# Kernel optimization log

Measured on AMD Instinct MI355X. Metric: run time of the kernel, lower is better.

The kernel has to match this reference:

```python
import jax, jax.numpy as jnp
import numpy as np

B_SCALE = 1.3195079565048218
N_LEVELS = 16
BASE_RES = 16
MAX_PARAMS = 2 ** 19
N_POINTS = 1048576
PRIMES = (1, 2654435761, 805459861)  # uint32 hash primes (Instant-NGP)


def _level_meta():
    offsets, sizes, inds = [], [], []
    off = 0
    for i in range(N_LEVELS):
        res = int(np.ceil(BASE_RES * np.exp(i * np.log(B_SCALE)) - 1.0)) + 1
        p = res ** 3
        if p % 8 != 0:
            p = ((p + 7) // 8) * 8
        p = min(MAX_PARAMS, p)
        offsets.append(off)
        sizes.append(p)
        inds.append(res ** 3 <= p)  # dense (under_hash) vs hashed level
        off += p
    return offsets, sizes, inds, off


OFFSETS, SIZES, INDICATORS, TOTAL_PARAMS = _level_meta()
TOTAL_HASH_SIZE = TOTAL_PARAMS * 2  # == 11445040


def _encode_level(x01, table2, level):
    # x01: [N,3] in [0,1]; table2: [total_params, 2]
    scale = np.float32(BASE_RES * np.exp(level * np.log(B_SCALE)) - 1.0)
    resolution = np.uint32(np.ceil(scale) + 1)
    map_size = np.uint32(SIZES[level])
    pos = x01 * scale + 0.5
    grid_f = jnp.floor(pos)
    frac = pos - grid_f                           # [N,3] trilinear weights
    grid = grid_f.astype(jnp.uint32)              # [N,3]
    feat = jnp.zeros((x01.shape[0], 2), dtype=table2.dtype)
    primes = np.array(PRIMES, dtype=np.uint32)
    stride = np.array([1, int(resolution), int(resolution) * int(resolution)], dtype=np.uint32)
    for idx in range(8):  # 8 grid corners
        sel = np.array([(idx >> d) & 1 for d in range(3)], dtype=np.uint32)
        corner = grid + sel                       # [N,3] uint32
        w = jnp.prod(jnp.where(sel[None, :] == 1, frac, 1.0 - frac), axis=-1)  # [N]
        if INDICATORS[level]:
            c = corner * stride[None, :]
            h = c[:, 0] + c[:, 1] + c[:, 2]       # under_hash (dense indexing)
        else:
            c = corner * primes[None, :]          # uint32 wraparound multiply
            h = c[:, 0] ^ c[:, 1] ^ c[:, 2]       # fast_hash
        index = (h % map_size).astype(jnp.int32) + np.int32(OFFSETS[level])
        feat = feat + w[:, None] * table2[index]  # gather + trilinear blend
    return feat


def setup_inputs() -> dict:
    key = jax.random.key(0)
    k1, k2 = jax.random.split(key)
    positions = jax.random.uniform(k1, (N_POINTS, 3), dtype=jnp.float32, minval=-1.0, maxval=1.0)
    # random_initialize: (rand*2-1)*1e-4
    hash_table = jax.random.uniform(k2, (TOTAL_HASH_SIZE,), dtype=jnp.float32, minval=-1e-4, maxval=1e-4)
    return {"positions": positions, "hash_table": hash_table}


def reference(positions, hash_table):
    x01 = (positions + 1.0) * 0.5  # bound = 1
    table2 = hash_table.reshape(-1, 2)
    feats = [_encode_level(x01, table2, l) for l in range(N_LEVELS)]
    return jnp.concatenate(feats, axis=-1)  # [N, 32]
```

## Files before the change

### kernel.cpp

```cpp
#include <hip/hip_runtime.h>
#include <math.h>
#include <stdint.h>

#define NLV 16
#define NDENSE 6
#define NHASH 10
#define NMERGE 6
#define SORT_RES 32
#define NBINS (SORT_RES * SORT_RES * SORT_RES)

typedef float evf2 __attribute__((ext_vector_type(2)));
typedef unsigned int evu4 __attribute__((ext_vector_type(4)));
typedef _Float16 evh2 __attribute__((ext_vector_type(2)));
typedef _Float16 evh4 __attribute__((ext_vector_type(4)));

struct Params {
  float scale[NLV];
  uint32_t res[NLV];
  uint32_t msize[NLV];
  uint32_t offset[NLV];
};

struct ParamsD {
  float scale[NDENSE];
  uint32_t res[NDENSE];
  uint32_t msize[NDENSE];
  uint32_t offset[NDENSE];
};

struct ParamsH {
  float scale[NMERGE];
  uint32_t offset[NMERGE];
};

__device__ __forceinline__ float ntload(const float* p) {
  return __builtin_nontemporal_load(p);
}

__device__ __forceinline__ int xcd_swz(int bid, int nwg) {
  int q = nwg >> 3, r = nwg & 7;
  int x = bid & 7, i = bid >> 3;
  return (x < r ? x * (q + 1) : r * (q + 1) + (x - r) * q) + i;
}

__device__ __forceinline__ uint32_t cell_key(float xr, float yr, float zr) {
  float x01 = (xr + 1.0f) * 0.5f;
  float y01 = (yr + 1.0f) * 0.5f;
  float z01 = (zr + 1.0f) * 0.5f;
  int cx = (int)(x01 * (float)SORT_RES);
  int cy = (int)(y01 * (float)SORT_RES);
  int cz = (int)(z01 * (float)SORT_RES);
  cx = cx < 0 ? 0 : (cx > SORT_RES-1 ? SORT_RES-1 : cx);
  cy = cy < 0 ? 0 : (cy > SORT_RES-1 ? SORT_RES-1 : cy);
  cz = cz < 0 ? 0 : (cz > SORT_RES-1 ? SORT_RES-1 : cz);
  return (uint32_t)(cx | (cy << 5) | (cz << 10));
}

__global__ __launch_bounds__(256) void zero_bins_kernel(uint32_t* bins) {
  int i = blockIdx.x * 256 + threadIdx.x;
  if (i < NBINS) bins[i] = 0u;
}

__global__ __launch_bounds__(256) void hist_kernel(
    const float* __restrict__ positions, uint32_t* __restrict__ bins, int n) {
  int t = blockIdx.x * 256 + threadIdx.x;
  int p0 = t * 4;
  if (p0 >= n) return;
  const float4 A = *reinterpret_cast<const float4*>(positions + 3*p0);
  const float4 B = *reinterpret_cast<const float4*>(positions + 3*p0 + 4);
  const float4 C = *reinterpret_cast<const float4*>(positions + 3*p0 + 8);
  atomicAdd(&bins[cell_key(A.x, A.y, A.z)], 1u);
  atomicAdd(&bins[cell_key(A.w, B.x, B.y)], 1u);
  atomicAdd(&bins[cell_key(B.z, B.w, C.x)], 1u);
  atomicAdd(&bins[cell_key(C.y, C.z, C.w)], 1u);
}

__global__ __launch_bounds__(1024) void scan_kernel(
    const uint32_t* __restrict__ bins, uint32_t* __restrict__ cursor) {
  __shared__ uint32_t lds[1024];
  int t = threadIdx.x;
  uint32_t local[32];
  uint32_t s = 0;
  #pragma unroll
  for (int j = 0; j < 32; ++j) { local[j] = bins[t*32 + j]; s += local[j]; }
  lds[t] = s;
  __syncthreads();
  for (int off = 1; off < 1024; off <<= 1) {
    uint32_t v = (t >= off) ? lds[t - off] : 0u;
    __syncthreads();
    lds[t] += v;
    __syncthreads();
  }
  uint32_t run = lds[t] - s;
  #pragma unroll
  for (int j = 0; j < 32; ++j) { cursor[t*32 + j] = run; run += local[j]; }
}

__global__ __launch_bounds__(256) void scatter_kernel(
    const float* __restrict__ positions, uint32_t* __restrict__ cursor,
    evu4* __restrict__ spi, int n) {
  int t = blockIdx.x * 256 + threadIdx.x;
  int p0 = t * 4;
  if (p0 >= n) return;
  const float4 A = *reinterpret_cast<const float4*>(positions + 3*p0);
  const float4 B = *reinterpret_cast<const float4*>(positions + 3*p0 + 4);
  const float4 C = *reinterpret_cast<const float4*>(positions + 3*p0 + 8);
  float xs[4] = {A.x, A.w, B.z, C.y};
  float ys[4] = {A.y, B.x, B.w, C.z};
  float zs[4] = {A.z, B.y, C.x, C.w};
  #pragma unroll
  for (int q = 0; q < 4; ++q) {
    uint32_t k = cell_key(xs[q], ys[q], zs[q]);
    uint32_t dst = atomicAdd(&cursor[k], 1u);
    evu4 v;
    v.x = __float_as_uint(xs[q]);
    v.y = __float_as_uint(ys[q]);
    v.z = __float_as_uint(zs[q]);
    v.w = (uint32_t)(p0 + q);
    spi[dst] = v;
  }
}

__device__ __forceinline__ void hash_feat(
    float x01, float y01, float z01, float scale, uint32_t mask,
    const float* __restrict__ tbl, float& f0, float& f1)
{
  float px = x01 * scale + 0.5f;
  float py = y01 * scale + 0.5f;
  float pz = z01 * scale + 0.5f;
  float fx = floorf(px), fy = floorf(py), fz = floorf(pz);
  float tx = px - fx, ty = py - fy, tz = pz - fz;
  uint32_t gx = (uint32_t)fx, gy = (uint32_t)fy, gz = (uint32_t)fz;

  float wxa = 1.0f - tx, wxb = tx;
  float wy_[2] = {1.0f - ty, ty};
  float wz_[2] = {1.0f - tz, tz};

  f0 = 0.0f; f1 = 0.0f;
  if ((gx & 1u) == 0u) {
    #pragma unroll
    for (int cyz = 0; cyz < 4; ++cyz) {
      uint32_t cy = gy + (cyz & 1u);
      uint32_t cz = gz + (cyz >> 1);
      uint32_t hy = (cy * 2654435761u) ^ (cz * 805459861u);
      uint32_t ha = (gx ^ hy) & mask;
      float wyz = wy_[cyz & 1u] * wz_[cyz >> 1];
      float wa = wxa * wyz, wb = wxb * wyz;
      const float4 t4 = *reinterpret_cast<const float4*>(tbl + 2u * (ha & ~1u));
      float2 ta, tb;
      if (ha & 1u) { ta.x = t4.z; ta.y = t4.w; tb.x = t4.x; tb.y = t4.y; }
      else         { ta.x = t4.x; ta.y = t4.y; tb.x = t4.z; tb.y = t4.w; }
      f0 += wa * ta.x; f1 += wa * ta.y;
      f0 += wb * tb.x; f1 += wb * tb.y;
    }
  } else {
    #pragma unroll
    for (int cyz = 0; cyz < 4; ++cyz) {
      uint32_t cy = gy + (cyz & 1u);
      uint32_t cz = gz + (cyz >> 1);
      uint32_t hy = (cy * 2654435761u) ^ (cz * 805459861u);
      uint32_t ha = (gx ^ hy) & mask;
      uint32_t hb = ((gx + 1u) ^ hy) & mask;
      float wyz = wy_[cyz & 1u] * wz_[cyz >> 1];
      float wa = wxa * wyz, wb = wxb * wyz;
      const float2 ta = *reinterpret_cast<const float2*>(tbl + 2u * ha);
      const float2 tb = *reinterpret_cast<const float2*>(tbl + 2u * hb);
      f0 += wa * ta.x; f1 += wa * ta.y;
      f0 += wb * tb.x; f1 += wb * tb.y;
    }
  }
}

__global__ __launch_bounds__(256) void hash_multi_kernel(
    const evu4* __restrict__ spi,
    const float* __restrict__ table,
    evh2* __restrict__ tmpH,
    ParamsH ph, uint32_t mask, int n)
{
  int bid = xcd_swz(blockIdx.x, gridDim.x);
  int t = bid * 256 + threadIdx.x;
  int p0 = t * 2;
  if (p0 >= n) return;

  evu4 a = __builtin_nontemporal_load(spi + p0);
  evu4 b = __builtin_nontemporal_load(spi + p0 + 1);
  float x0 = (__uint_as_float(a.x) + 1.0f) * 0.5f;
  float y0 = (__uint_as_float(a.y) + 1.0f) * 0.5f;
  float z0 = (__uint_as_float(a.z) + 1.0f) * 0.5f;
  float x1 = (__uint_as_float(b.x) + 1.0f) * 0.5f;
  float y1 = (__uint_as_float(b.y) + 1.0f) * 0.5f;
  float z1 = (__uint_as_float(b.z) + 1.0f) * 0.5f;

  #pragma unroll
  for (int l = 0; l < NMERGE; ++l) {
    const float s = ph.scale[l];
    const float* __restrict__ tbl = table + 2u * ph.offset[l];
    float f00, f01, f10, f11;
    hash_feat(x0, y0, z0, s, mask, tbl, f00, f01);
    hash_feat(x1, y1, z1, s, mask, tbl, f10, f11);
    evh4 v;
    v.x = (_Float16)f00; v.y = (_Float16)f01;
    v.z = (_Float16)f10; v.w = (_Float16)f11;
    __builtin_nontemporal_store(v,
        reinterpret_cast<evh4*>(tmpH + (size_t)l * n + p0));
  }
}

__global__ __launch_bounds__(256) void hash_level_kernel(
    const evu4* __restrict__ spi,
    const float* __restrict__ tbl,
    evh2* __restrict__ tmpH,
    float scale, uint32_t mask, int n)
{
  int bid = xcd_swz(blockIdx.x, gridDim.x);
  int t = bid * 256 + threadIdx.x;
  int p0 = t * 2;
  if (p0 >= n) return;

  evu4 a = __builtin_nontemporal_load(spi + p0);
  evu4 b = __builtin_nontemporal_load(spi + p0 + 1);
  float f00, f01, f10, f11;
  hash_feat((__uint_as_float(a.x) + 1.0f) * 0.5f,
            (__uint_as_float(a.y) + 1.0f) * 0.5f,
            (__uint_as_float(a.z) + 1.0f) * 0.5f, scale, mask, tbl, f00, f01);
  hash_feat((__uint_as_float(b.x) + 1.0f) * 0.5f,
            (__uint_as_float(b.y) + 1.0f) * 0.5f,
            (__uint_as_float(b.z) + 1.0f) * 0.5f, scale, mask, tbl, f10, f11);
  evh4 v;
  v.x = (_Float16)f00; v.y = (_Float16)f01;
  v.z = (_Float16)f10; v.w = (_Float16)f11;
  __builtin_nontemporal_store(v, reinterpret_cast<evh4*>(tmpH + p0));
}

#define PBS 128
__global__ __launch_bounds__(PBS) void dense_pack2_kernel(
    const evu4* __restrict__ spi,
    const float* __restrict__ table,
    const evh2* __restrict__ tmpH,
    float* __restrict__ out,
    ParamsD prm, int n)
{
  __shared__ float lds[PBS * 33];
  __shared__ uint32_t lds_oi[PBS];
  int t = threadIdx.x;
  int base = xcd_swz(blockIdx.x, gridDim.x) * PBS;
  int p = base + t;

  if (p < n) {
    evu4 a = __builtin_nontemporal_load(spi + p);
    float x = (__uint_as_float(a.x) + 1.0f) * 0.5f;
    float y = (__uint_as_float(a.y) + 1.0f) * 0.5f;
    float z = (__uint_as_float(a.z) + 1.0f) * 0.5f;
    lds_oi[t] = a.w;

    #pragma unroll
    for (int l = 0; l < NDENSE; ++l) {
      const float s = prm.scale[l];
      const uint32_t res = prm.res[l];
      const uint32_t ms = prm.msize[l];
      const float* __restrict__ tbl = table + 2u * prm.offset[l];
      const uint32_t res2 = res * res;

      float px = x * s + 0.5f;
      float py = y * s + 0.5f;
      float pz = z * s + 0.5f;
      float fx = floorf(px), fy = floorf(py), fz = floorf(pz);
      float tx = px - fx, ty = py - fy, tz = pz - fz;
      uint32_t gx = (uint32_t)fx, gy = (uint32_t)fy, gz = (uint32_t)fz;

      float wxa = 1.0f - tx, wxb = tx;
      float wy_[2] = {1.0f - ty, ty};
      float wz_[2] = {1.0f - tz, tz};

      float f0 = 0.0f, f1 = 0.0f;
      #pragma unroll
      for (int cyz = 0; cyz < 4; ++cyz) {
        uint32_t cy = gy + (cyz & 1u);
        uint32_t cz = gz + ((cyz >> 1) & 1u);
        uint32_t h = gx + cy * res + cz * res2;
        if (h >= ms) h -= ms;
        float wyz = wy_[cyz & 1u] * wz_[(cyz >> 1) & 1u];
        float2 ta, tb;
        if (h + 1u < ms) {
          const float4 t4 = *reinterpret_cast<const float4*>(tbl + 2u * h);
          ta.x = t4.x; ta.y = t4.y; tb.x = t4.z; tb.y = t4.w;
        } else {
          ta = *reinterpret_cast<const float2*>(tbl + 2u * h);
          tb = *reinterpret_cast<const float2*>(tbl);
        }
        float wa = wxa * wyz, wb = wxb * wyz;
        f0 += wa * ta.x; f1 += wa * ta.y;
        f0 += wb * tb.x; f1 += wb * tb.y;
      }
      lds[t*33 + 2*l]     = f0;
      lds[t*33 + 2*l + 1] = f1;
    }

    #pragma unroll
    for (int j = 0; j < NHASH; ++j) {
      evh2 v = __builtin_nontemporal_load(tmpH + (size_t)j * n + p);
      lds[t*33 + 12 + 2*j]     = (float)v.x;
      lds[t*33 + 12 + 2*j + 1] = (float)v.y;
    }
  }
  __syncthreads();

  if (base + PBS <= n) {
    int qr = t >> 3, r = t & 7;
    #pragma unroll
    for (int k = 0; k < 8; ++k) {
      int q = k * (PBS/8) + qr;
      uint32_t oi = lds_oi[q];
      float4 v = make_float4(lds[q*33 + r*4], lds[q*33 + r*4 + 1],
                             lds[q*33 + r*4 + 2], lds[q*33 + r*4 + 3]);
      reinterpret_cast<float4*>(out + (size_t)oi * 32u)[r] = v;
    }
  } else if (p < n) {
    uint32_t oi = lds_oi[t];
    float4* o = reinterpret_cast<float4*>(out + (size_t)oi * 32u);
    #pragma unroll
    for (int k = 0; k < 8; ++k)
      o[k] = make_float4(lds[t*33 + 4*k], lds[t*33 + 4*k + 1],
                         lds[t*33 + 4*k + 2], lds[t*33 + 4*k + 3]);
  }
}

__global__ __launch_bounds__(256) void hash_enc_kernel(
    const float* __restrict__ positions,
    const float* __restrict__ table,
    float* __restrict__ out,
    Params prm, int n)
{
  int p = blockIdx.x * 256 + threadIdx.x;
  if (p >= n) return;

  float x = (positions[3*p+0] + 1.0f) * 0.5f;
  float y = (positions[3*p+1] + 1.0f) * 0.5f;
  float z = (positions[3*p+2] + 1.0f) * 0.5f;

  float acc[32];

  #pragma unroll
  for (int l = 0; l < NLV; ++l) {
    const float s = prm.scale[l];
    const uint32_t res = prm.res[l];
    const uint32_t ms = prm.msize[l];
    const uint32_t off = prm.offset[l];
    float px = x * s + 0.5f;
    float py = y * s + 0.5f;
    float pz = z * s + 0.5f;
    float fx = floorf(px), fy = floorf(py), fz = floorf(pz);
    float tx = px - fx, ty = py - fy, tz = pz - fz;
    uint32_t gx = (uint32_t)fx, gy = (uint32_t)fy, gz = (uint32_t)fz;
    float wx[2] = {1.0f - tx, tx};
    float wy[2] = {1.0f - ty, ty};
    float wz[2] = {1.0f - tz, tz};
    float f0 = 0.0f, f1 = 0.0f;
    #pragma unroll
    for (int c = 0; c < 8; ++c) {
      uint32_t cx = gx + (c & 1u);
      uint32_t cy = gy + ((c >> 1) & 1u);
      uint32_t cz = gz + ((c >> 2) & 1u);
      uint32_t h;
      if (l < NDENSE) {
        h = cx + cy * res + cz * res * res;
        if (h >= ms) h -= ms;
      } else {
        h = cx ^ (cy * 2654435761u) ^ (cz * 805459861u);
        h &= (ms - 1u);
      }
      float w = (wx[c & 1u] * wy[(c >> 1) & 1u]) * wz[(c >> 2) & 1u];
      const float2 t = *reinterpret_cast<const float2*>(table + 2u * (h + off));
      f0 += w * t.x;
      f1 += w * t.y;
    }
    acc[2*l]   = f0;
    acc[2*l+1] = f1;
  }

  float4* o = reinterpret_cast<float4*>(out + (size_t)p * 32u);
  #pragma unroll
  for (int k = 0; k < 8; ++k)
    o[k] = make_float4(acc[4*k+0], acc[4*k+1], acc[4*k+2], acc[4*k+3]);
}

extern "C" void kernel_launch(void* const* d_in, const int* in_sizes, int n_in,
                              void* d_out, int out_size, void* d_ws, size_t ws_size,
                              hipStream_t stream) {
  const float* positions = (const float*)d_in[0];
  const float* table     = (const float*)d_in[1];
  float* out             = (float*)d_out;
  int n = in_sizes[0] / 3;

  Params prm;
  const double lnb = log(1.3195079565048218);
  uint32_t off = 0;
  for (int l = 0; l < NLV; ++l) {
    double sd = 16.0 * exp((double)l * lnb) - 1.0;
    uint32_t res_meta = (uint32_t)ceil(sd) + 1u;
    uint64_t p3 = (uint64_t)res_meta * res_meta * res_meta;
    uint64_t ps = (p3 % 8ull) ? ((p3 + 7ull) / 8ull) * 8ull : p3;
    if (ps > (1ull << 19)) ps = 1ull << 19;
    float sf = (float)sd;
    uint32_t res_enc = (uint32_t)(ceilf(sf) + 1.0f);
    prm.scale[l]  = sf;
    prm.res[l]    = res_enc;
    prm.msize[l]  = (uint32_t)ps;
    prm.offset[l] = off;
    off += (uint32_t)ps;
  }
  ParamsD pd;
  for (int l = 0; l < NDENSE; ++l) {
    pd.scale[l] = prm.scale[l]; pd.res[l] = prm.res[l];
    pd.msize[l] = prm.msize[l]; pd.offset[l] = prm.offset[l];
  }
  ParamsH ph;
  for (int l = 0; l < NMERGE; ++l) {
    ph.scale[l]  = prm.scale[NDENSE + l];
    ph.offset[l] = prm.offset[NDENSE + l];
  }

  dim3 block(256);
  dim3 gfull((n + 255) / 256);
  dim3 ghash((n/2 + 255) / 256);
  dim3 gquad((n/4 + 255) / 256);
  dim3 gpack((n + PBS - 1) / PBS);

  size_t tmp_b  = (size_t)NHASH * n * sizeof(evh2);
  size_t sp_off = tmp_b;
  size_t bn_off = sp_off + (size_t)n * sizeof(evu4);
  size_t cu_off = bn_off + (size_t)NBINS * sizeof(uint32_t);
  size_t total  = cu_off + (size_t)NBINS * sizeof(uint32_t);

  char* wsb = (char*)d_ws;

  if (ws_size >= total && (n % 4) == 0) {
    evh2*     tmpH   = (evh2*)wsb;
    evu4*     spi    = (evu4*)(wsb + sp_off);
    uint32_t* bins   = (uint32_t*)(wsb + bn_off);
    uint32_t* cursor = (uint32_t*)(wsb + cu_off);

    hipLaunchKernelGGL(zero_bins_kernel, dim3((NBINS + 255) / 256), block, 0, stream, bins);
    hipLaunchKernelGGL(hist_kernel, gquad, block, 0, stream, positions, bins, n);
    hipLaunchKernelGGL(scan_kernel, dim3(1), dim3(1024), 0, stream, bins, cursor);
    hipLaunchKernelGGL(scatter_kernel, gquad, block, 0, stream,
                       positions, cursor, spi, n);

    hipLaunchKernelGGL(hash_multi_kernel, ghash, block, 0, stream,
                       spi, table, tmpH, ph, prm.msize[NDENSE] - 1u, n);
    for (int l = NDENSE + NMERGE; l < NLV; ++l) {
      hipLaunchKernelGGL(hash_level_kernel, ghash, block, 0, stream,
                         spi, table + 2u * prm.offset[l],
                         tmpH + (size_t)(l - NDENSE) * n,
                         prm.scale[l], prm.msize[l] - 1u, n);
    }
    hipLaunchKernelGGL(dense_pack2_kernel, gpack, dim3(PBS), 0, stream,
                       spi, table, tmpH, out, pd, n);
  } else {
    hipLaunchKernelGGL(hash_enc_kernel, gfull, block, 0, stream,
                       positions, table, out, prm, n);
  }
}
```

Baseline: 432.6 us.

## Fuse last four hashed levels into one kernel, simplify scatter, stream output

Replaces the four separate per-level launches for the finest hashed levels with a single kernel that loops over those levels, reusing the loaded sorted positions and cutting launch and re-read overhead. The scatter kernel now handles one point per thread instead of four, which raises thread count and atomic parallelism but drops the vectorized position loads. The dense pack kernel's final output writes become nontemporal stores. The merged kernel holds more live state per thread and serializes four levels of gathers inside one thread, which may lower occupancy and reduce latency hiding.

```diff
diff --git a/kernel.cpp b/kernel.cpp
--- a/kernel.cpp
+++ b/kernel.cpp
@@ -6,10 +6,12 @@
 #define NDENSE 6
 #define NHASH 10
 #define NMERGE 6
+#define NMERGE2 4
 #define SORT_RES 32
 #define NBINS (SORT_RES * SORT_RES * SORT_RES)
 
 typedef float evf2 __attribute__((ext_vector_type(2)));
+typedef float evf4 __attribute__((ext_vector_type(4)));
 typedef unsigned int evu4 __attribute__((ext_vector_type(4)));
 typedef _Float16 evh2 __attribute__((ext_vector_type(2)));
 typedef _Float16 evh4 __attribute__((ext_vector_type(4)));
@@ -33,9 +35,10 @@
   uint32_t offset[NMERGE];
 };
 
-__device__ __forceinline__ float ntload(const float* p) {
-  return __builtin_nontemporal_load(p);
-}
+struct ParamsH2 {
+  float scale[NMERGE2];
+  uint32_t offset[NMERGE2];
+};
 
 __device__ __forceinline__ int xcd_swz(int bid, int nwg) {
   int q = nwg >> 3, r = nwg & 7;
@@ -99,26 +102,17 @@
 __global__ __launch_bounds__(256) void scatter_kernel(
     const float* __restrict__ positions, uint32_t* __restrict__ cursor,
     evu4* __restrict__ spi, int n) {
-  int t = blockIdx.x * 256 + threadIdx.x;
-  int p0 = t * 4;
-  if (p0 >= n) return;
-  const float4 A = *reinterpret_cast<const float4*>(positions + 3*p0);
-  const float4 B = *reinterpret_cast<const float4*>(positions + 3*p0 + 4);
-  const float4 C = *reinterpret_cast<const float4*>(positions + 3*p0 + 8);
-  float xs[4] = {A.x, A.w, B.z, C.y};
-  float ys[4] = {A.y, B.x, B.w, C.z};
-  float zs[4] = {A.z, B.y, C.x, C.w};
-  #pragma unroll
-  for (int q = 0; q < 4; ++q) {
-    uint32_t k = cell_key(xs[q], ys[q], zs[q]);
-    uint32_t dst = atomicAdd(&cursor[k], 1u);
-    evu4 v;
-    v.x = __float_as_uint(xs[q]);
-    v.y = __float_as_uint(ys[q]);
-    v.z = __float_as_uint(zs[q]);
-    v.w = (uint32_t)(p0 + q);
-    spi[dst] = v;
-  }
+  int p = blockIdx.x * 256 + threadIdx.x;
+  if (p >= n) return;
+  float x = positions[3*p], y = positions[3*p+1], z = positions[3*p+2];
+  uint32_t k = cell_key(x, y, z);
+  uint32_t dst = atomicAdd(&cursor[k], 1u);
+  evu4 v;
+  v.x = __float_as_uint(x);
+  v.y = __float_as_uint(y);
+  v.z = __float_as_uint(z);
+  v.w = (uint32_t)p;
+  spi[dst] = v;
 }
 
 __device__ __forceinline__ void hash_feat(
@@ -206,11 +200,11 @@
   }
 }
 
-__global__ __launch_bounds__(256) void hash_level_kernel(
+__global__ __launch_bounds__(256) void hash_multi2_kernel(
     const evu4* __restrict__ spi,
-    const float* __restrict__ tbl,
+    const float* __restrict__ table,
     evh2* __restrict__ tmpH,
-    float scale, uint32_t mask, int n)
+    ParamsH2 ph, uint32_t mask, int n)
 {
   int bid = xcd_swz(blockIdx.x, gridDim.x);
   int t = bid * 256 + threadIdx.x;
@@ -219,17 +213,26 @@
 
   evu4 a = __builtin_nontemporal_load(spi + p0);
   evu4 b = __builtin_nontemporal_load(spi + p0 + 1);
-  float f00, f01, f10, f11;
-  hash_feat((__uint_as_float(a.x) + 1.0f) * 0.5f,
-            (__uint_as_float(a.y) + 1.0f) * 0.5f,
-            (__uint_as_float(a.z) + 1.0f) * 0.5f, scale, mask, tbl, f00, f01);
-  hash_feat((__uint_as_float(b.x) + 1.0f) * 0.5f,
-            (__uint_as_float(b.y) + 1.0f) * 0.5f,
-            (__uint_as_float(b.z) + 1.0f) * 0.5f, scale, mask, tbl, f10, f11);
-  evh4 v;
-  v.x = (_Float16)f00; v.y = (_Float16)f01;
-  v.z = (_Float16)f10; v.w = (_Float16)f11;
-  __builtin_nontemporal_store(v, reinterpret_cast<evh4*>(tmpH + p0));
+  float x0 = (__uint_as_float(a.x) + 1.0f) * 0.5f;
+  float y0 = (__uint_as_float(a.y) + 1.0f) * 0.5f;
+  float z0 = (__uint_as_float(a.z) + 1.0f) * 0.5f;
+  float x1 = (__uint_as_float(b.x) + 1.0f) * 0.5f;
+  float y1 = (__uint_as_float(b.y) + 1.0f) * 0.5f;
+  float z1 = (__uint_as_float(b.z) + 1.0f) * 0.5f;
+
+  #pragma unroll
+  for (int l = 0; l < NMERGE2; ++l) {
+    const float s = ph.scale[l];
+    const float* __restrict__ tbl = table + 2u * ph.offset[l];
+    float f00, f01, f10, f11;
+    hash_feat(x0, y0, z0, s, mask, tbl, f00, f01);
+    hash_feat(x1, y1, z1, s, mask, tbl, f10, f11);
+    evh4 v;
+    v.x = (_Float16)f00; v.y = (_Float16)f01;
+    v.z = (_Float16)f10; v.w = (_Float16)f11;
+    __builtin_nontemporal_store(v,
+        reinterpret_cast<evh4*>(tmpH + (size_t)(NMERGE + l) * n + p0));
+  }
 }
 
 #define PBS 128
@@ -311,9 +314,11 @@
     for (int k = 0; k < 8; ++k) {
       int q = k * (PBS/8) + qr;
       uint32_t oi = lds_oi[q];
-      float4 v = make_float4(lds[q*33 + r*4], lds[q*33 + r*4 + 1],
-                             lds[q*33 + r*4 + 2], lds[q*33 + r*4 + 3]);
-      reinterpret_cast<float4*>(out + (size_t)oi * 32u)[r] = v;
+      evf4 v;
+      v.x = lds[q*33 + r*4];     v.y = lds[q*33 + r*4 + 1];
+      v.z = lds[q*33 + r*4 + 2]; v.w = lds[q*33 + r*4 + 3];
+      __builtin_nontemporal_store(v,
+          reinterpret_cast<evf4*>(out + (size_t)oi * 32u) + r);
     }
   } else if (p < n) {
     uint32_t oi = lds_oi[t];
@@ -419,6 +424,11 @@
     ph.scale[l]  = prm.scale[NDENSE + l];
     ph.offset[l] = prm.offset[NDENSE + l];
   }
+  ParamsH2 ph2;
+  for (int l = 0; l < NMERGE2; ++l) {
+    ph2.scale[l]  = prm.scale[NDENSE + NMERGE + l];
+    ph2.offset[l] = prm.offset[NDENSE + NMERGE + l];
+  }
 
   dim3 block(256);
   dim3 gfull((n + 255) / 256);
@@ -443,17 +453,13 @@
     hipLaunchKernelGGL(zero_bins_kernel, dim3((NBINS + 255) / 256), block, 0, stream, bins);
     hipLaunchKernelGGL(hist_kernel, gquad, block, 0, stream, positions, bins, n);
     hipLaunchKernelGGL(scan_kernel, dim3(1), dim3(1024), 0, stream, bins, cursor);
-    hipLaunchKernelGGL(scatter_kernel, gquad, block, 0, stream,
+    hipLaunchKernelGGL(scatter_kernel, gfull, block, 0, stream,
                        positions, cursor, spi, n);
 
     hipLaunchKernelGGL(hash_multi_kernel, ghash, block, 0, stream,
                        spi, table, tmpH, ph, prm.msize[NDENSE] - 1u, n);
-    for (int l = NDENSE + NMERGE; l < NLV; ++l) {
-      hipLaunchKernelGGL(hash_level_kernel, ghash, block, 0, stream,
-                         spi, table + 2u * prm.offset[l],
-                         tmpH + (size_t)(l - NDENSE) * n,
-                         prm.scale[l], prm.msize[l] - 1u, n);
-    }
+    hipLaunchKernelGGL(hash_multi2_kernel, ghash, block, 0, stream,
+                       spi, table, tmpH, ph2, prm.msize[NDENSE] - 1u, n);
     hipLaunchKernelGGL(dense_pack2_kernel, gpack, dim3(PBS), 0, stream,
                        spi, table, tmpH, out, pd, n);
   } else {
```

Result: slower. 501.0 us (+15.8%).
